# Performance work log

Hardware: AMD Instinct MI355X
Metric: run time of the kernel (lower is better)

The kernel has to match this reference:

```python
import jax, jax.numpy as jnp
import numpy as np

SCALE = 0.08838834764831845  # 1/sqrt(128)
NEG_INF = -1e30


def setup_inputs() -> dict:
    key = jax.random.key(0)
    ks = jax.random.split(key, 6)
    S, Hq, Hkv, D, NB, BS, BMAX, X = 32, 32, 8, 128, 4096, 16, 128, 8
    query = jax.random.normal(ks[0], (S, Hq, D), jnp.float32)
    key_cache = jax.random.normal(ks[1], (NB, Hkv, D // X, BS, X), jnp.float32)
    value_cache = jax.random.normal(ks[2], (NB, Hkv, D, BS), jnp.float32)
    block_tables = jax.random.randint(ks[3], (S, BMAX), 0, NB, dtype=jnp.int32)
    seq_lens = jax.random.randint(ks[4], (S,), 1, BMAX * BS + 1, dtype=jnp.int32)
    alibi_slopes = jax.random.uniform(ks[5], (Hq,), jnp.float32)
    query_start_len = jnp.arange(S + 1, dtype=jnp.int32)  # every seq is a 1-token decode
    return dict(query_ptr=query, key_cache_ptr=key_cache, value_cache_ptr=value_cache,
                block_tables_ptr=block_tables, seq_lens_ptr=seq_lens,
                alibi_slopes_ptr=alibi_slopes, query_start_len_ptr=query_start_len)


def reference(query_ptr, key_cache_ptr, value_cache_ptr, block_tables_ptr,
              seq_lens_ptr, alibi_slopes_ptr, query_start_len_ptr):
    S, Bmax = block_tables_ptr.shape
    NB, Hkv, D0, BS, X = key_cache_ptr.shape
    D = D0 * X
    Hq = query_ptr.shape[1]
    G = Hq // Hkv  # queries per kv head
    Kmax = Bmax * BS

    # de-interleave vLLM K layout [NB,Hkv,D//x,BS,x] -> [NB,Hkv,BS,D]; K[d] = cache[.., d//x, tok, d%x]
    K = key_cache_ptr.transpose(0, 1, 3, 2, 4).reshape(NB, Hkv, BS, D).astype(jnp.float32)
    V = value_cache_ptr.transpose(0, 1, 3, 2).astype(jnp.float32)  # [NB,Hkv,BS,D]

    qstart = query_start_len_ptr[:-1]
    qlen = query_start_len_ptr[1:] - qstart

    q = query_ptr[qstart].astype(jnp.float32).reshape(S, Hkv, G, D)  # one decode token per seq

    # block-table-driven KV gather: [S,Bmax,Hkv,BS,D] -> [S,Hkv,Kmax,D]
    Kg = K[block_tables_ptr].transpose(0, 2, 1, 3, 4).reshape(S, Hkv, Kmax, D)
    Vg = V[block_tables_ptr].transpose(0, 2, 1, 3, 4).reshape(S, Hkv, Kmax, D)

    scores = SCALE * jnp.einsum('shgd,shkd->shgk', q, Kg)  # [S,Hkv,G,Kmax]

    pos = jnp.arange(Kmax, dtype=jnp.float32)
    ctx = (seq_lens_ptr.astype(jnp.float32) - 1.0)[:, None, None, None]
    slopes = alibi_slopes_ptr.reshape(Hkv, G)  # head idx = kv_head*G + q
    bias = slopes[None, :, :, None] * (pos[None, None, None, :] - ctx)
    valid = (jnp.arange(Kmax)[None, :] < seq_lens_ptr[:, None])[:, None, None, :]
    scores = jnp.where(valid, scores + bias, NEG_INF)

    m = jnp.max(scores, axis=-1, keepdims=True)
    p = jnp.exp(scores - m) * valid  # online-softmax numerator
    l = jnp.sum(p, axis=-1, keepdims=True)
    acc = jnp.einsum('shgk,shkd->shgd', p, Vg)
    out = acc / (l + 1e-10)  # matches acc/(L + 1e-10) in source

    decode = (qlen == 1).astype(query_ptr.dtype)  # seqs with query_len>1 are skipped (zeros)
    out = out.reshape(S, Hq, D).astype(query_ptr.dtype) * decode[:, None, None]
    return jnp.zeros_like(query_ptr).at[qstart].set(out)
```

## Files before the change

### kernel.cpp

```cpp
#include <hip/hip_runtime.h>

#define SCALE_F 0.08838834764831845f
#define NEG_INF -1e30f

constexpr int S    = 32;
constexpr int Hq   = 32;
constexpr int Hkv  = 8;
constexpr int G    = 4;
constexpr int D    = 128;
constexpr int BS   = 16;
constexpr int BMAX = 128;
constexpr int KMAX = BMAX * BS;

__global__ __launch_bounds__(256, 4)
void attn_part_kernel(const float* __restrict__ q_ptr,
                      const float* __restrict__ kc,
                      const float* __restrict__ vc,
                      const int*   __restrict__ bt,
                      const int*   __restrict__ slens,
                      const float* __restrict__ slopes,
                      float* __restrict__ part_acc,
                      float* __restrict__ part_m,
                      float* __restrict__ part_l,
                      int parts, int chunk)
{
    extern __shared__ float smem[];
    float* sm_s   = smem;
    float* sm_acc = smem + G * chunk;

    const int bid  = blockIdx.x;
    const int part = bid % parts;
    const int sh   = bid / parts;
    const int h    = sh % Hkv;
    const int s    = sh / Hkv;

    const int seq_len   = slens[s];
    const int num_parts = (seq_len + chunk - 1) / chunk;
    if (part >= num_parts) return;

    const int tid      = threadIdx.x;
    const int cpb      = chunk / BS;
    const int kvb0     = part * cpb;
    const int nb_total = (seq_len + BS - 1) / BS;

    float slope[G];
    #pragma unroll
    for (int g = 0; g < G; ++g) slope[g] = slopes[h * G + g];
    const float ctx = (float)(seq_len - 1);

    const int o = tid >> 4;
    const int t = tid & 15;

    float4 qa[G], qb[G];
    #pragma unroll
    for (int g = 0; g < G; ++g) {
        const float* qp = q_ptr + ((size_t)(s * Hq + h * G + g) * D + t * 8);
        qa[g] = ((const float4*)qp)[0];
        qb[g] = ((const float4*)qp)[1];
    }

    for (int i = 0; i < cpb; ++i) {
        const int kvb = kvb0 + i;
        float sc[G];
        if (kvb < nb_total) {
            const int phys = bt[s * BMAX + kvb];
            const float* kp = kc + ((((size_t)phys * Hkv + h) * (D / 8) + t) * BS + o) * 8;
            float4 ka = ((const float4*)kp)[0];
            float4 kb = ((const float4*)kp)[1];
            #pragma unroll
            for (int g = 0; g < G; ++g) {
                sc[g] = qa[g].x * ka.x + qa[g].y * ka.y + qa[g].z * ka.z + qa[g].w * ka.w
                      + qb[g].x * kb.x + qb[g].y * kb.y + qb[g].z * kb.z + qb[g].w * kb.w;
            }
            #pragma unroll
            for (int g = 0; g < G; ++g) {
                #pragma unroll
                for (int msk = 8; msk >= 1; msk >>= 1)
                    sc[g] += __shfl_xor(sc[g], msk, 16);
            }
            const int kpos = kvb * BS + o;
            const bool valid = kpos < seq_len;
            #pragma unroll
            for (int g = 0; g < G; ++g)
                sc[g] = valid ? (SCALE_F * sc[g] + slope[g] * ((float)kpos - ctx)) : NEG_INF;
        } else {
            #pragma unroll
            for (int g = 0; g < G; ++g) sc[g] = NEG_INF;
        }
        if (t == 0) {
            #pragma unroll
            for (int g = 0; g < G; ++g) sm_s[g * chunk + i * BS + o] = sc[g];
        }
    }
    __syncthreads();

    {
        const int g    = tid >> 6;
        const int lane = tid & 63;
        float m = NEG_INF;
        for (int j = lane; j < chunk; j += 64) m = fmaxf(m, sm_s[g * chunk + j]);
        #pragma unroll
        for (int msk = 32; msk >= 1; msk >>= 1) m = fmaxf(m, __shfl_xor(m, msk, 64));
        float l = 0.f;
        for (int j = lane; j < chunk; j += 64) {
            float p = __expf(sm_s[g * chunk + j] - m);
            sm_s[g * chunk + j] = p;
            l += p;
        }
        #pragma unroll
        for (int msk = 32; msk >= 1; msk >>= 1) l += __shfl_xor(l, msk, 64);
        if (lane == 0) {
            part_m[(sh * parts + part) * G + g] = m;
            part_l[(sh * parts + part) * G + g] = l;
        }
    }
    __syncthreads();

    const int d    = tid & 127;
    const int half = tid >> 7;
    float acc[G] = {0.f, 0.f, 0.f, 0.f};
    const int cpb_valid = min(cpb, nb_total - kvb0);
    for (int i = half; i < cpb_valid; i += 2) {
        const int phys = bt[s * BMAX + kvb0 + i];
        const float* vp = vc + (((size_t)phys * Hkv + h) * D + d) * BS;
        float4 v0 = ((const float4*)vp)[0];
        float4 v1 = ((const float4*)vp)[1];
        float4 v2 = ((const float4*)vp)[2];
        float4 v3 = ((const float4*)vp)[3];
        #pragma unroll
        for (int g = 0; g < G; ++g) {
            const float4* pp = (const float4*)(sm_s + g * chunk + i * BS);
            float4 p0 = pp[0], p1 = pp[1], p2 = pp[2], p3 = pp[3];
            acc[g] += p0.x * v0.x + p0.y * v0.y + p0.z * v0.z + p0.w * v0.w;
            acc[g] += p1.x * v1.x + p1.y * v1.y + p1.z * v1.z + p1.w * v1.w;
            acc[g] += p2.x * v2.x + p2.y * v2.y + p2.z * v2.z + p2.w * v2.w;
            acc[g] += p3.x * v3.x + p3.y * v3.y + p3.z * v3.z + p3.w * v3.w;
        }
    }
    if (half == 1) {
        #pragma unroll
        for (int g = 0; g < G; ++g) sm_acc[g * D + d] = acc[g];
    }
    __syncthreads();
    if (half == 0) {
        float* outp = part_acc + (size_t)(sh * parts + part) * G * D;
        #pragma unroll
        for (int g = 0; g < G; ++g)
            outp[g * D + d] = acc[g] + sm_acc[g * D + d];
    }
}

__global__ __launch_bounds__(512)
void attn_reduce_kernel(const float* __restrict__ part_acc,
                        const float* __restrict__ part_m,
                        const float* __restrict__ part_l,
                        const int*   __restrict__ slens,
                        float* __restrict__ out,
                        int parts, int chunk)
{
    const int sh  = blockIdx.x;
    const int s   = sh / Hkv;
    const int tid = threadIdx.x;
    const int g   = tid >> 7;
    const int d   = tid & 127;

    const int seq_len = slens[s];
    const int np = min(parts, (seq_len + chunk - 1) / chunk);

    float M = NEG_INF;
    for (int p = 0; p < np; ++p)
        M = fmaxf(M, part_m[(sh * parts + p) * G + g]);
    float L = 0.f, acc = 0.f;
    for (int p = 0; p < np; ++p) {
        const float w = __expf(part_m[(sh * parts + p) * G + g] - M);
        L += w * part_l[(sh * parts + p) * G + g];
        acc += w * part_acc[((size_t)(sh * parts + p) * G + g) * D + d];
    }
    out[(size_t)(sh * G + g) * D + d] = acc / (L + 1e-10f);
}

extern "C" void kernel_launch(void* const* d_in, const int* in_sizes, int n_in,
                              void* d_out, int out_size, void* d_ws, size_t ws_size,
                              hipStream_t stream)
{
    const float* q   = (const float*)d_in[0];
    const float* kc  = (const float*)d_in[1];
    const float* vc  = (const float*)d_in[2];
    const int*   bt  = (const int*)d_in[3];
    const int*   sl  = (const int*)d_in[4];
    const float* slp = (const float*)d_in[5];

    int parts = 8;
    while (parts > 1 &&
           (size_t)S * Hkv * parts * G * (D + 2) * sizeof(float) > ws_size)
        parts >>= 1;
    const int chunk = KMAX / parts;

    float* part_acc = (float*)d_ws;
    float* part_m   = part_acc + (size_t)S * Hkv * parts * G * D;
    float* part_l   = part_m   + (size_t)S * Hkv * parts * G;

    const size_t lds = (size_t)(G * chunk + G * D) * sizeof(float);

    attn_part_kernel<<<S * Hkv * parts, 256, lds, stream>>>(
        q, kc, vc, bt, sl, slp, part_acc, part_m, part_l, parts, chunk);
    attn_reduce_kernel<<<S * Hkv, 512, 0, stream>>>(
        part_acc, part_m, part_l, sl, (float*)d_out, parts, chunk);
}
```

Measured before the change: 492.1 us.

## Template split-K kernel on parts, prefetch K/V blocks, raise split to 16

Makes the partition count a template parameter so the chunk size and LDS arrays are known at compile time. The block-table entries are preloaded into registers, and the next K and V blocks are register double-buffered so their global loads overlap with compute. The softmax loops are bounded to the valid length, the default split rises from 8 to 16 parts, and the occupancy hint goes from 4 to 6. The cost is more register pressure from the prefetch buffers and the phys array, plus more partial results for the reduce kernel to combine.

```diff
diff --git a/kernel.cpp b/kernel.cpp
--- a/kernel.cpp
+++ b/kernel.cpp
@@ -12,7 +12,8 @@
 constexpr int BMAX = 128;
 constexpr int KMAX = BMAX * BS;
 
-__global__ __launch_bounds__(256, 4)
+template<int PARTS>
+__global__ __launch_bounds__(256, 6)
 void attn_part_kernel(const float* __restrict__ q_ptr,
                       const float* __restrict__ kc,
                       const float* __restrict__ vc,
@@ -21,32 +22,38 @@
                       const float* __restrict__ slopes,
                       float* __restrict__ part_acc,
                       float* __restrict__ part_m,
-                      float* __restrict__ part_l,
-                      int parts, int chunk)
+                      float* __restrict__ part_l)
 {
-    extern __shared__ float smem[];
-    float* sm_s   = smem;
-    float* sm_acc = smem + G * chunk;
+    constexpr int CHUNK = KMAX / PARTS;
+    constexpr int CPB   = CHUNK / BS;
+
+    __shared__ float sm_s[G * CHUNK];
+    __shared__ float sm_acc[G * D];
 
     const int bid  = blockIdx.x;
-    const int part = bid % parts;
-    const int sh   = bid / parts;
+    const int part = bid % PARTS;
+    const int sh   = bid / PARTS;
     const int h    = sh % Hkv;
     const int s    = sh / Hkv;
 
     const int seq_len   = slens[s];
-    const int num_parts = (seq_len + chunk - 1) / chunk;
+    const int num_parts = (seq_len + CHUNK - 1) / CHUNK;
     if (part >= num_parts) return;
 
-    const int tid      = threadIdx.x;
-    const int cpb      = chunk / BS;
-    const int kvb0     = part * cpb;
-    const int nb_total = (seq_len + BS - 1) / BS;
+    const int tid       = threadIdx.x;
+    const int kvb0      = part * CPB;
+    const int nb_total  = (seq_len + BS - 1) / BS;
+    const int cpb_valid = min(CPB, nb_total - kvb0);
+    const int lim       = cpb_valid * BS;
 
     float slope[G];
     #pragma unroll
     for (int g = 0; g < G; ++g) slope[g] = slopes[h * G + g];
     const float ctx = (float)(seq_len - 1);
+
+    int phys[CPB];
+    #pragma unroll
+    for (int i = 0; i < CPB; ++i) phys[i] = bt[s * BMAX + kvb0 + i];
 
     const int o = tid >> 4;
     const int t = tid & 15;
@@ -59,38 +66,40 @@
         qb[g] = ((const float4*)qp)[1];
     }
 
-    for (int i = 0; i < cpb; ++i) {
-        const int kvb = kvb0 + i;
+    float4 ka, kb, nka, nkb;
+    {
+        const float* kp = kc + ((((size_t)phys[0] * Hkv + h) * (D / 8) + t) * BS + o) * 8;
+        ka = ((const float4*)kp)[0];
+        kb = ((const float4*)kp)[1];
+    }
+    #pragma unroll
+    for (int i = 0; i < CPB; ++i) {
+        if (i >= cpb_valid) break;
+        if (i + 1 < cpb_valid) {
+            const float* kp = kc + ((((size_t)phys[i + 1] * Hkv + h) * (D / 8) + t) * BS + o) * 8;
+            nka = ((const float4*)kp)[0];
+            nkb = ((const float4*)kp)[1];
+        }
         float sc[G];
-        if (kvb < nb_total) {
-            const int phys = bt[s * BMAX + kvb];
-            const float* kp = kc + ((((size_t)phys * Hkv + h) * (D / 8) + t) * BS + o) * 8;
-            float4 ka = ((const float4*)kp)[0];
-            float4 kb = ((const float4*)kp)[1];
+        #pragma unroll
+        for (int g = 0; g < G; ++g)
+            sc[g] = qa[g].x * ka.x + qa[g].y * ka.y + qa[g].z * ka.z + qa[g].w * ka.w
+                  + qb[g].x * kb.x + qb[g].y * kb.y + qb[g].z * kb.z + qb[g].w * kb.w;
+        #pragma unroll
+        for (int g = 0; g < G; ++g) {
             #pragma unroll
-            for (int g = 0; g < G; ++g) {
-                sc[g] = qa[g].x * ka.x + qa[g].y * ka.y + qa[g].z * ka.z + qa[g].w * ka.w
-                      + qb[g].x * kb.x + qb[g].y * kb.y + qb[g].z * kb.z + qb[g].w * kb.w;
-            }
-            #pragma unroll
-            for (int g = 0; g < G; ++g) {
-                #pragma unroll
-                for (int msk = 8; msk >= 1; msk >>= 1)
-                    sc[g] += __shfl_xor(sc[g], msk, 16);
-            }
-            const int kpos = kvb * BS + o;
-            const bool valid = kpos < seq_len;
+            for (int msk = 8; msk >= 1; msk >>= 1)
+                sc[g] += __shfl_xor(sc[g], msk, 16);
+        }
+        const int kpos  = (kvb0 + i) * BS + o;
+        const bool valid = kpos < seq_len;
+        if (t == 0) {
             #pragma unroll
             for (int g = 0; g < G; ++g)
-                sc[g] = valid ? (SCALE_F * sc[g] + slope[g] * ((float)kpos - ctx)) : NEG_INF;
-        } else {
-            #pragma unroll
-            for (int g = 0; g < G; ++g) sc[g] = NEG_INF;
-        }
-        if (t == 0) {
-            #pragma unroll
-            for (int g = 0; g < G; ++g) sm_s[g * chunk + i * BS + o] = sc[g];
-        }
+                sm_s[g * CHUNK + i * BS + o] =
+                    valid ? (SCALE_F * sc[g] + slope[g] * ((float)kpos - ctx)) : NEG_INF;
+        }
+        ka = nka; kb = nkb;
     }
     __syncthreads();
 
@@ -98,20 +107,20 @@
         const int g    = tid >> 6;
         const int lane = tid & 63;
         float m = NEG_INF;
-        for (int j = lane; j < chunk; j += 64) m = fmaxf(m, sm_s[g * chunk + j]);
+        for (int j = lane; j < lim; j += 64) m = fmaxf(m, sm_s[g * CHUNK + j]);
         #pragma unroll
         for (int msk = 32; msk >= 1; msk >>= 1) m = fmaxf(m, __shfl_xor(m, msk, 64));
         float l = 0.f;
-        for (int j = lane; j < chunk; j += 64) {
-            float p = __expf(sm_s[g * chunk + j] - m);
-            sm_s[g * chunk + j] = p;
+        for (int j = lane; j < lim; j += 64) {
+            float p = __expf(sm_s[g * CHUNK + j] - m);
+            sm_s[g * CHUNK + j] = p;
             l += p;
         }
         #pragma unroll
         for (int msk = 32; msk >= 1; msk >>= 1) l += __shfl_xor(l, msk, 64);
         if (lane == 0) {
-            part_m[(sh * parts + part) * G + g] = m;
-            part_l[(sh * parts + part) * G + g] = l;
+            part_m[(sh * PARTS + part) * G + g] = m;
+            part_l[(sh * PARTS + part) * G + g] = l;
         }
     }
     __syncthreads();
@@ -119,23 +128,29 @@
     const int d    = tid & 127;
     const int half = tid >> 7;
     float acc[G] = {0.f, 0.f, 0.f, 0.f};
-    const int cpb_valid = min(cpb, nb_total - kvb0);
+
+    float4 v0, v1, v2, v3, w0, w1, w2, w3;
+    if (half < cpb_valid) {
+        const float* vp = vc + (((size_t)phys[half] * Hkv + h) * D + d) * BS;
+        v0 = ((const float4*)vp)[0]; v1 = ((const float4*)vp)[1];
+        v2 = ((const float4*)vp)[2]; v3 = ((const float4*)vp)[3];
+    }
     for (int i = half; i < cpb_valid; i += 2) {
-        const int phys = bt[s * BMAX + kvb0 + i];
-        const float* vp = vc + (((size_t)phys * Hkv + h) * D + d) * BS;
-        float4 v0 = ((const float4*)vp)[0];
-        float4 v1 = ((const float4*)vp)[1];
-        float4 v2 = ((const float4*)vp)[2];
-        float4 v3 = ((const float4*)vp)[3];
+        if (i + 2 < cpb_valid) {
+            const float* vp = vc + (((size_t)phys[i + 2] * Hkv + h) * D + d) * BS;
+            w0 = ((const float4*)vp)[0]; w1 = ((const float4*)vp)[1];
+            w2 = ((const float4*)vp)[2]; w3 = ((const float4*)vp)[3];
+        }
         #pragma unroll
         for (int g = 0; g < G; ++g) {
-            const float4* pp = (const float4*)(sm_s + g * chunk + i * BS);
+            const float4* pp = (const float4*)(sm_s + g * CHUNK + i * BS);
             float4 p0 = pp[0], p1 = pp[1], p2 = pp[2], p3 = pp[3];
             acc[g] += p0.x * v0.x + p0.y * v0.y + p0.z * v0.z + p0.w * v0.w;
             acc[g] += p1.x * v1.x + p1.y * v1.y + p1.z * v1.z + p1.w * v1.w;
             acc[g] += p2.x * v2.x + p2.y * v2.y + p2.z * v2.z + p2.w * v2.w;
             acc[g] += p3.x * v3.x + p3.y * v3.y + p3.z * v3.z + p3.w * v3.w;
         }
+        v0 = w0; v1 = w1; v2 = w2; v3 = w3;
     }
     if (half == 1) {
         #pragma unroll
@@ -143,7 +158,7 @@
     }
     __syncthreads();
     if (half == 0) {
-        float* outp = part_acc + (size_t)(sh * parts + part) * G * D;
+        float* outp = part_acc + (size_t)(sh * PARTS + part) * G * D;
         #pragma unroll
         for (int g = 0; g < G; ++g)
             outp[g * D + d] = acc[g] + sm_acc[g * D + d];
@@ -190,20 +205,25 @@
     const int*   sl  = (const int*)d_in[4];
     const float* slp = (const float*)d_in[5];
 
-    int parts = 8;
-    while (parts > 1 &&
-           (size_t)S * Hkv * parts * G * (D + 2) * sizeof(float) > ws_size)
-        parts >>= 1;
+    auto ws_need = [](int p) {
+        return (size_t)S * Hkv * p * G * (D + 2) * sizeof(float);
+    };
+    int parts = 16;
+    while (parts > 1 && ws_need(parts) > ws_size) parts >>= 1;
     const int chunk = KMAX / parts;
 
     float* part_acc = (float*)d_ws;
     float* part_m   = part_acc + (size_t)S * Hkv * parts * G * D;
     float* part_l   = part_m   + (size_t)S * Hkv * parts * G;
 
-    const size_t lds = (size_t)(G * chunk + G * D) * sizeof(float);
-
-    attn_part_kernel<<<S * Hkv * parts, 256, lds, stream>>>(
-        q, kc, vc, bt, sl, slp, part_acc, part_m, part_l, parts, chunk);
+    const dim3 grid1(S * Hkv * parts);
+    switch (parts) {
+    case 16: attn_part_kernel<16><<<grid1, 256, 0, stream>>>(q, kc, vc, bt, sl, slp, part_acc, part_m, part_l); break;
+    case 8:  attn_part_kernel<8> <<<grid1, 256, 0, stream>>>(q, kc, vc, bt, sl, slp, part_acc, part_m, part_l); break;
+    case 4:  attn_part_kernel<4> <<<grid1, 256, 0, stream>>>(q, kc, vc, bt, sl, slp, part_acc, part_m, part_l); break;
+    case 2:  attn_part_kernel<2> <<<grid1, 256, 0, stream>>>(q, kc, vc, bt, sl, slp, part_acc, part_m, part_l); break;
+    default: attn_part_kernel<1> <<<grid1, 256, 0, stream>>>(q, kc, vc, bt, sl, slp, part_acc, part_m, part_l); break;
+    }
     attn_reduce_kernel<<<S * Hkv, 512, 0, stream>>>(
         part_acc, part_m, part_l, sl, (float*)d_out, parts, chunk);
 }
```

New measurement: 476.6 us. -3.2%, faster.
